# Kernel optimization log

Hardware: AMD Instinct MI355X
Metric: run time of the kernel (lower is better)

The kernel has to match this reference:

```python
import jax, jax.numpy as jnp
import numpy as np

VOCAB = 32000; DIM = 512; NL = 6; B = 2; L = 1024
DI = 2 * DIM      # d_inner (expand=2)
DS = 16           # d_state
DC = 4            # d_conv
DR = DIM // 16    # dt_rank = ceil(512/16) = 32


def setup_inputs() -> dict:
    key = jax.random.key(0)
    ks = jax.random.split(key, 10)
    s = 0.02
    tokens = jax.random.randint(ks[0], (B, L), 0, VOCAB)
    pos_emb = jax.random.normal(ks[1], (1, L, DIM)) * s
    embed = jax.random.normal(ks[2], (VOCAB, DIM)) * s
    lm_w = jax.random.normal(ks[3], (VOCAB, DIM)) * s
    lm_b = jnp.zeros((VOCAB,), jnp.float32)
    in_proj_w = jax.random.normal(ks[4], (NL, 2 * DI, DIM)) * s
    conv_w = jax.random.normal(ks[5], (NL, DI, DC)) * s
    conv_b = jnp.zeros((NL, DI), jnp.float32)
    x_proj_w = jax.random.normal(ks[6], (NL, DR + 2 * DS, DI)) * s
    dt_proj_w = jax.random.normal(ks[7], (NL, DI, DR)) * s
    dt_proj_b = jnp.broadcast_to(jnp.log(jnp.expm1(jnp.float32(0.01))), (NL, DI)).astype(jnp.float32)
    A_log = jnp.log(jnp.broadcast_to(jnp.arange(1, DS + 1, dtype=jnp.float32), (NL, DI, DS)))
    Dp = jnp.ones((NL, DI), jnp.float32)
    out_w = jax.random.normal(ks[8], (NL, DIM, DI)) * s
    ln_g = jnp.ones((NL, DIM), jnp.float32)
    ln_b = jnp.zeros((NL, DIM), jnp.float32)
    return dict(tokens=tokens, pos_emb=pos_emb, embed=embed, lm_w=lm_w, lm_b=lm_b,
                in_proj_w=in_proj_w, conv_w=conv_w, conv_b=conv_b, x_proj_w=x_proj_w,
                dt_proj_w=dt_proj_w, dt_proj_b=dt_proj_b, A_log=A_log, Dp=Dp,
                out_w=out_w, ln_g=ln_g, ln_b=ln_b)


def silu(x):
    return x * jax.nn.sigmoid(x)


def layernorm(x, g, b, eps=1e-5):
    mu = jnp.mean(x, -1, keepdims=True)
    var = jnp.var(x, -1, keepdims=True)
    return (x - mu) * jax.lax.rsqrt(var + eps) * g + b


def causal_dwconv(x, w, b):
    # x: (B,L,DI), w: (DI,DC) depthwise, left-pad causal
    xp = jnp.pad(x, ((0, 0), (DC - 1, 0), (0, 0)))
    y = b
    for k in range(DC):
        y = y + w[:, k] * xp[:, k:k + x.shape[1], :]
    return y


def selective_scan(u, dt, A, Bm, Cm, Dp):
    # u,dt: (B,L,DI); A: (DI,DS); Bm,Cm: (B,L,DS)
    dA = jnp.exp(dt[..., None] * A)                       # (B,L,DI,DS)
    dBu = dt[..., None] * Bm[:, :, None, :] * u[..., None]
    h0 = jnp.zeros((u.shape[0], DI, DS), u.dtype)

    def step(h, inp):
        dA_t, dBu_t, C_t = inp
        h = dA_t * h + dBu_t
        y = jnp.einsum('bdn,bn->bd', h, C_t)
        return h, y

    _, ys = jax.lax.scan(step, h0, (dA.transpose(1, 0, 2, 3),
                                    dBu.transpose(1, 0, 2, 3),
                                    Cm.transpose(1, 0, 2)))
    return ys.transpose(1, 0, 2) + u * Dp


def mamba_block(x, in_w, cw, cb, xp_w, dtw, dtb, A_log, Dp, ow):
    xz = jnp.einsum('bld,ed->ble', x, in_w)               # (B,L,2*DI)
    xc, z = jnp.split(xz, 2, axis=-1)
    xc = silu(causal_dwconv(xc, cw, cb))
    x_dbl = jnp.einsum('bld,ed->ble', xc, xp_w)           # (B,L,DR+2*DS)
    dt, Bm, Cm = jnp.split(x_dbl, [DR, DR + DS], axis=-1)
    dt = jax.nn.softplus(jnp.einsum('blr,dr->bld', dt, dtw) + dtb)
    A = -jnp.exp(A_log)
    y = selective_scan(xc, dt, A, Bm, Cm, Dp)
    y = y * silu(z)
    return jnp.einsum('bld,ed->ble', y, ow)


def reference(tokens, pos_emb, embed, lm_w, lm_b, in_proj_w, conv_w, conv_b,
              x_proj_w, dt_proj_w, dt_proj_b, A_log, Dp, out_w, ln_g, ln_b):
    x = embed[tokens] + pos_emb[:, :tokens.shape[1]]
    for i in range(NL):
        res = x
        x = mamba_block(x, in_proj_w[i], conv_w[i], conv_b[i], x_proj_w[i],
                        dt_proj_w[i], dt_proj_b[i], A_log[i], Dp[i], out_w[i])
        x = layernorm(x + res, ln_g[i], ln_b[i])
    return jnp.einsum('bld,vd->blv', x, lm_w) + lm_b
```

## Files before the change

kernel.cpp:

```cpp
#include <hip/hip_runtime.h>
#include <hip/hip_bf16.h>
#include <math.h>

#define BB 2
#define LL 1024
#define DIM 512
#define NL 6
#define DI 1024
#define DS 16
#define DC 4
#define DR 32
#define VOCAB 32000
#define M_ROWS (BB * LL)
#define CCH 64
#define CHLEN (LL / CCH)
#define KSPLIT 8
#define OSPLIT 4

typedef unsigned short u16;
typedef __attribute__((ext_vector_type(8))) short bf16x8;
typedef __attribute__((ext_vector_type(4))) float f32x4;

__device__ __forceinline__ u16 f2bf(float f) {
    unsigned u = __float_as_uint(f);
    u += 0x7FFF + ((u >> 16) & 1);
    return (u16)(u >> 16);
}
__device__ __forceinline__ float bf2f(u16 h) {
    return __uint_as_float(((unsigned)h) << 16);
}
#define SWZ(r, c) ((c) ^ (((r) >> 1) & 3))

__global__ __launch_bounds__(256) void cast_all(const float* __restrict__ lm,
                                                const float* __restrict__ inw,
                                                const float* __restrict__ ow,
                                                const float* __restrict__ xp,
                                                u16* __restrict__ lmb,
                                                u16* __restrict__ inb,
                                                u16* __restrict__ owb_,
                                                u16* __restrict__ xpb) {
    int idx = blockIdx.x * 256 + threadIdx.x;
    const float* src; u16* dst; int off;
    if (idx < 2048000)      { src = lm;  dst = lmb;  off = idx; }
    else if (idx < 2834432) { src = inw; dst = inb;  off = idx - 2048000; }
    else if (idx < 3227648) { src = ow;  dst = owb_; off = idx - 2834432; }
    else                    { src = xp;  dst = xpb;  off = idx - 3227648; }
    float4 v0 = ((const float4*)src)[off * 2];
    float4 v1 = ((const float4*)src)[off * 2 + 1];
    union { u16 h[8]; int4 v; } r;
    r.h[0] = f2bf(v0.x); r.h[1] = f2bf(v0.y); r.h[2] = f2bf(v0.z); r.h[3] = f2bf(v0.w);
    r.h[4] = f2bf(v1.x); r.h[5] = f2bf(v1.y); r.h[6] = f2bf(v1.z); r.h[7] = f2bf(v1.w);
    ((int4*)dst)[off] = r.v;
}

__global__ __launch_bounds__(256) void embed_kernel(const int* __restrict__ tok,
                                                    const float* __restrict__ pos,
                                                    const float* __restrict__ emb,
                                                    float* __restrict__ x,
                                                    u16* __restrict__ xb) {
    int idx = blockIdx.x * 256 + threadIdx.x;
    int d = idx & (DIM - 1);
    int l = (idx >> 9) & (LL - 1);
    int b = idx >> 19;
    int t = tok[b * LL + l];
    float v = emb[(size_t)t * DIM + d] + pos[l * DIM + d];
    x[idx] = v;
    xb[idx] = f2bf(v);
}

__global__ __launch_bounds__(256) void gemm_bf16(const u16* __restrict__ A,
                                                 const u16* __restrict__ W,
                                                 const float* __restrict__ bias,
                                                 float* __restrict__ C,
                                                 int M, int N, int K,
                                                 int lda, int ldw) {
    __shared__ __align__(16) u16 As[2 * 4096];
    __shared__ __align__(16) u16 Ws[2 * 4096];
    const int t = threadIdx.x;
    const int l = t & 63;
    const int w = t >> 6;
    const int nwg = gridDim.x;
    const int q = nwg >> 3, r8 = nwg & 7;
    const int xcd = blockIdx.x & 7, rank = blockIdx.x >> 3;
    const int wgid = (xcd < r8 ? xcd * (q + 1) : r8 * (q + 1) + (xcd - r8) * q) + rank;
    const int Mb = M >> 7;
    const int bm = (wgid % Mb) * 128;
    const int bn = (wgid / Mb) * 128;
    const int wm = (w >> 1) * 64;
    const int wn = (w & 1) * 64;

    f32x4 acc[4][4] = {};
    const int nt = K >> 5;

    auto STAGE = [&](int bufi, int k0) {
#pragma unroll
        for (int p = 0; p < 2; ++p) {
            const int i = (p * 4 + w) * 64 + l;
            const int row = i >> 2;
            const int kq = SWZ(row, i & 3);
            __builtin_amdgcn_global_load_lds(
                (const __attribute__((address_space(1))) unsigned int*)
                    (A + (size_t)(bm + row) * lda + k0 + kq * 8),
                (__attribute__((address_space(3))) unsigned int*)
                    (As + bufi * 4096 + (p * 4 + w) * 512),
                16, 0, 0);
            __builtin_amdgcn_global_load_lds(
                (const __attribute__((address_space(1))) unsigned int*)
                    (W + (size_t)(bn + row) * ldw + k0 + kq * 8),
                (__attribute__((address_space(3))) unsigned int*)
                    (Ws + bufi * 4096 + (p * 4 + w) * 512),
                16, 0, 0);
        }
    };
    auto COMPUTE = [&](int bufi) {
        const u16* Ab = As + bufi * 4096;
        const u16* Wb = Ws + bufi * 4096;
#pragma unroll
        for (int mi = 0; mi < 4; ++mi) {
            const int ar = wm + mi * 16 + (l & 15);
            bf16x8 a = *(const bf16x8*)(Ab + ar * 32 + SWZ(ar, l >> 4) * 8);
#pragma unroll
            for (int ni = 0; ni < 4; ++ni) {
                const int wr = wn + ni * 16 + (l & 15);
                bf16x8 b = *(const bf16x8*)(Wb + wr * 32 + SWZ(wr, l >> 4) * 8);
                acc[mi][ni] = __builtin_amdgcn_mfma_f32_16x16x32_bf16(b, a, acc[mi][ni], 0, 0, 0);
            }
        }
    };

    STAGE(0, 0);
    for (int tt = 0; tt < nt; ++tt) {
        if (tt + 1 < nt) {
            STAGE((tt + 1) & 1, (tt + 1) << 5);
            asm volatile("s_waitcnt vmcnt(4)\ns_barrier" ::: "memory");
        } else {
            asm volatile("s_waitcnt vmcnt(0)\ns_barrier" ::: "memory");
        }
        COMPUTE(tt & 1);
        asm volatile("s_waitcnt lgkmcnt(0)\ns_barrier" ::: "memory");
    }

#pragma unroll
    for (int mi = 0; mi < 4; ++mi) {
        const int row = bm + wm + mi * 16 + (l & 15);
#pragma unroll
        for (int ni = 0; ni < 4; ++ni) {
            const int col = bn + wn + ni * 16 + ((l >> 4) << 2);
            float4 v;
            v.x = acc[mi][ni][0]; v.y = acc[mi][ni][1];
            v.z = acc[mi][ni][2]; v.w = acc[mi][ni][3];
            if (bias != nullptr) {
                float4 b4 = *(const float4*)(bias + col);
                v.x += b4.x; v.y += b4.y; v.z += b4.z; v.w += b4.w;
            }
            *(float4*)(C + (size_t)row * N + col) = v;
        }
    }
}

__global__ __launch_bounds__(256) void gemm_n64(const u16* __restrict__ A,
                                                const u16* __restrict__ W,
                                                float* __restrict__ out,
                                                u16* __restrict__ outb,
                                                int lda, int ldw, int ldc,
                                                int KS, int pstride) {
    __shared__ __align__(16) u16 As[2 * 4096];
    __shared__ __align__(16) u16 Ws[2 * 2048];
    const int t = threadIdx.x;
    const int l = t & 63;
    const int w = t >> 6;
    const int kz = blockIdx.x;
    const int bm = blockIdx.y * 128;
    const int bnn = blockIdx.z * 64;
    const int wm = w * 32;

    f32x4 acc[2][4] = {};
    const int nt = KS >> 5;
    const int kbeg = kz * KS;

    auto STAGE = [&](int bufi, int k0) {
#pragma unroll
        for (int p = 0; p < 2; ++p) {
            const int i = p * 256 + w * 64 + l;
            const int row = i >> 2;
            const int kq = SWZ(row, i & 3);
            __builtin_amdgcn_global_load_lds(
                (const __attribute__((address_space(1))) unsigned int*)
                    (A + (size_t)(bm + row) * lda + k0 + kq * 8),
                (__attribute__((address_space(3))) unsigned int*)
                    (As + bufi * 4096 + (p * 256 + w * 64) * 8),
                16, 0, 0);
        }
        {
            const int i = w * 64 + l;
            const int row = i >> 2;
            const int kq = SWZ(row, i & 3);
            __builtin_amdgcn_global_load_lds(
                (const __attribute__((address_space(1))) unsigned int*)
                    (W + (size_t)(bnn + row) * ldw + k0 + kq * 8),
                (__attribute__((address_space(3))) unsigned int*)
                    (Ws + bufi * 2048 + (w * 64) * 8),
                16, 0, 0);
        }
    };
    auto COMPUTE = [&](int bufi) {
        const u16* Ab = As + bufi * 4096;
        const u16* Wb = Ws + bufi * 2048;
#pragma unroll
        for (int mi = 0; mi < 2; ++mi) {
            const int ar = wm + mi * 16 + (l & 15);
            bf16x8 a = *(const bf16x8*)(Ab + ar * 32 + SWZ(ar, l >> 4) * 8);
#pragma unroll
            for (int ni = 0; ni < 4; ++ni) {
                const int wr = ni * 16 + (l & 15);
                bf16x8 b = *(const bf16x8*)(Wb + wr * 32 + SWZ(wr, l >> 4) * 8);
                acc[mi][ni] = __builtin_amdgcn_mfma_f32_16x16x32_bf16(b, a, acc[mi][ni], 0, 0, 0);
            }
        }
    };

    STAGE(0, kbeg);
    for (int tt = 0; tt < nt; ++tt) {
        if (tt + 1 < nt) {
            STAGE((tt + 1) & 1, kbeg + ((tt + 1) << 5));
            asm volatile("s_waitcnt vmcnt(3)\ns_barrier" ::: "memory");
        } else {
            asm volatile("s_waitcnt vmcnt(0)\ns_barrier" ::: "memory");
        }
        COMPUTE(tt & 1);
        asm volatile("s_waitcnt lgkmcnt(0)\ns_barrier" ::: "memory");
    }

    if (outb != nullptr) {
        u16* opb = outb + (size_t)kz * pstride;
#pragma unroll
        for (int mi = 0; mi < 2; ++mi) {
            const int row = bm + wm + mi * 16 + (l & 15);
#pragma unroll
            for (int ni = 0; ni < 4; ++ni) {
                const int col = bnn + ni * 16 + ((l >> 4) << 2);
                ushort4 v;
                v.x = f2bf(acc[mi][ni][0]); v.y = f2bf(acc[mi][ni][1]);
                v.z = f2bf(acc[mi][ni][2]); v.w = f2bf(acc[mi][ni][3]);
                *(ushort4*)(opb + (size_t)row * ldc + col) = v;
            }
        }
    } else {
        float* op = out + (size_t)kz * pstride;
#pragma unroll
        for (int mi = 0; mi < 2; ++mi) {
            const int row = bm + wm + mi * 16 + (l & 15);
#pragma unroll
            for (int ni = 0; ni < 4; ++ni) {
                const int col = bnn + ni * 16 + ((l >> 4) << 2);
                float4 v;
                v.x = acc[mi][ni][0]; v.y = acc[mi][ni][1];
                v.z = acc[mi][ni][2]; v.w = acc[mi][ni][3];
                *(float4*)(op + (size_t)row * ldc + col) = v;
            }
        }
    }
}

__global__ __launch_bounds__(256) void xdred_dt(const float* __restrict__ Pf,
                                                const float* __restrict__ dtw,
                                                const float* __restrict__ dtb,
                                                float* __restrict__ xd,
                                                float* __restrict__ dt) {
    __shared__ float xds[64];
    const int m = blockIdx.x;
    const int t = threadIdx.x;
    if (t < 64) {
        float s = 0.f;
#pragma unroll
        for (int kz = 0; kz < KSPLIT; ++kz)
            s += Pf[(size_t)kz * (M_ROWS * 64) + m * 64 + t];
        xds[t] = s;
        xd[m * 64 + t] = s;
    }
    __syncthreads();
    const int d0 = t * 4;
    const float4 bv = *(const float4*)(dtb + d0);
    float a0 = bv.x, a1 = bv.y, a2 = bv.z, a3 = bv.w;
    const float* w0p = dtw + (size_t)(d0 + 0) * DR;
    const float* w1p = dtw + (size_t)(d0 + 1) * DR;
    const float* w2p = dtw + (size_t)(d0 + 2) * DR;
    const float* w3p = dtw + (size_t)(d0 + 3) * DR;
#pragma unroll
    for (int k = 0; k < DR; k += 4) {
        float4 xv = *(const float4*)&xds[k];
        float4 w0 = *(const float4*)(w0p + k);
        float4 w1 = *(const float4*)(w1p + k);
        float4 w2 = *(const float4*)(w2p + k);
        float4 w3 = *(const float4*)(w3p + k);
        a0 += w0.x * xv.x + w0.y * xv.y + w0.z * xv.z + w0.w * xv.w;
        a1 += w1.x * xv.x + w1.y * xv.y + w1.z * xv.z + w1.w * xv.w;
        a2 += w2.x * xv.x + w2.y * xv.y + w2.z * xv.z + w2.w * xv.w;
        a3 += w3.x * xv.x + w3.y * xv.y + w3.z * xv.z + w3.w * xv.w;
    }
    a0 = (a0 > 20.f) ? a0 : log1pf(__expf(a0));
    a1 = (a1 > 20.f) ? a1 : log1pf(__expf(a1));
    a2 = (a2 > 20.f) ? a2 : log1pf(__expf(a2));
    a3 = (a3 > 20.f) ? a3 : log1pf(__expf(a3));
    float4 v; v.x = a0; v.y = a1; v.z = a2; v.w = a3;
    *(float4*)(dt + (size_t)m * DI + d0) = v;
}

__global__ __launch_bounds__(256) void conv_silu(const u16* __restrict__ xzb,
                                                 const float* __restrict__ cw,
                                                 const float* __restrict__ cb,
                                                 float* __restrict__ xc,
                                                 u16* __restrict__ xcb) {
    int idx = blockIdx.x * 256 + threadIdx.x;
    int c = idx & (DI - 1);
    int l = (idx >> 10) & (LL - 1);
    int b = idx >> 20;
    float acc = cb[c];
#pragma unroll
    for (int k = 0; k < DC; ++k) {
        int ll = l + k - (DC - 1);
        if (ll >= 0)
            acc += cw[c * DC + k] * bf2f(xzb[((size_t)(b * LL + ll)) * (2 * DI) + c]);
    }
    float v = acc / (1.f + __expf(-acc));
    xc[idx] = v;
    xcb[idx] = f2bf(v);
}

__global__ __launch_bounds__(256) void scan_pass1(const float* __restrict__ xc,
                                                  const float* __restrict__ dt,
                                                  const float* __restrict__ xdbl,
                                                  const float* __restrict__ A_log,
                                                  float* __restrict__ S,
                                                  float* __restrict__ Q) {
    const int d = blockIdx.x * 256 + threadIdx.x;
    const int b = blockIdx.y;
    const int c = blockIdx.z;
    float a[DS];
#pragma unroll
    for (int q = 0; q < 4; ++q) {
        float4 al = *(const float4*)(A_log + d * DS + q * 4);
        a[q * 4 + 0] = -__expf(al.x);
        a[q * 4 + 1] = -__expf(al.y);
        a[q * 4 + 2] = -__expf(al.z);
        a[q * 4 + 3] = -__expf(al.w);
    }
    float Qr[DS];
#pragma unroll
    for (int n = 0; n < DS; ++n) Qr[n] = 0.f;
    float Ssum = 0.f;

    const int l0 = c * CHLEN;
    const float* dtp = dt + ((size_t)b * LL + l0) * DI + d;
    const float* up  = xc + ((size_t)b * LL + l0) * DI + d;
    const float* xdp = xdbl + ((size_t)b * LL + l0) * 64 + DR;

    for (int l = 0; l < CHLEN; ++l) {
        float dtv = dtp[(size_t)l * DI];
        float uv  = up[(size_t)l * DI];
        float wv = dtv * uv;
        Ssum += dtv;
#pragma unroll
        for (int q = 0; q < 4; ++q) {
            float4 Bv = *(const float4*)(xdp + l * 64 + q * 4);
            float dA0 = __expf(dtv * a[q * 4 + 0]);
            float dA1 = __expf(dtv * a[q * 4 + 1]);
            float dA2 = __expf(dtv * a[q * 4 + 2]);
            float dA3 = __expf(dtv * a[q * 4 + 3]);
            Qr[q * 4 + 0] = dA0 * Qr[q * 4 + 0] + wv * Bv.x;
            Qr[q * 4 + 1] = dA1 * Qr[q * 4 + 1] + wv * Bv.y;
            Qr[q * 4 + 2] = dA2 * Qr[q * 4 + 2] + wv * Bv.z;
            Qr[q * 4 + 3] = dA3 * Qr[q * 4 + 3] + wv * Bv.w;
        }
    }
    S[((size_t)b * CCH + c) * DI + d] = Ssum;
    float* Qp = Q + (((size_t)b * CCH + c) * DI + d) * DS;
#pragma unroll
    for (int q = 0; q < 4; ++q) {
        float4 o;
        o.x = Qr[q * 4 + 0]; o.y = Qr[q * 4 + 1];
        o.z = Qr[q * 4 + 2]; o.w = Qr[q * 4 + 3];
        *(float4*)(Qp + q * 4) = o;
    }
}

__global__ __launch_bounds__(64) void scan_pass2(const float* __restrict__ A_log,
                                                 const float* __restrict__ S,
                                                 float* __restrict__ Q) {
    const int idx = blockIdx.x * 64 + threadIdx.x;
    const int b = idx >> 14;
    const int dn = idx & 16383;
    const int d = dn >> 4;
    const float a = -__expf(A_log[dn]);
    float h = 0.f;
    for (int c = 0; c < CCH; ++c) {
        const size_t soff = ((size_t)b * CCH + c) * DI + d;
        const size_t qoff = ((size_t)b * CCH + c) * (size_t)(DI * DS) + dn;
        float P = __expf(a * S[soff]);
        float qv = Q[qoff];
        Q[qoff] = h;
        h = P * h + qv;
    }
}

__global__ __launch_bounds__(256) void scan_pass3(const float* __restrict__ xc,
                                                  const float* __restrict__ dt,
                                                  const float* __restrict__ xdbl,
                                                  const u16* __restrict__ xzb,
                                                  const float* __restrict__ A_log,
                                                  const float* __restrict__ Dpp,
                                                  const float* __restrict__ Q,
                                                  u16* __restrict__ y) {
    const int d = blockIdx.x * 256 + threadIdx.x;
    const int b = blockIdx.y;
    const int c = blockIdx.z;
    float a[DS];
#pragma unroll
    for (int q = 0; q < 4; ++q) {
        float4 al = *(const float4*)(A_log + d * DS + q * 4);
        a[q * 4 + 0] = -__expf(al.x);
        a[q * 4 + 1] = -__expf(al.y);
        a[q * 4 + 2] = -__expf(al.z);
        a[q * 4 + 3] = -__expf(al.w);
    }
    float h[DS];
    const float* Qp = Q + (((size_t)b * CCH + c) * DI + d) * DS;
#pragma unroll
    for (int q = 0; q < 4; ++q) {
        float4 hv = *(const float4*)(Qp + q * 4);
        h[q * 4 + 0] = hv.x; h[q * 4 + 1] = hv.y;
        h[q * 4 + 2] = hv.z; h[q * 4 + 3] = hv.w;
    }
    const float dp = Dpp[d];

    const int l0 = c * CHLEN;
    const float* dtp = dt + ((size_t)b * LL + l0) * DI + d;
    const float* up  = xc + ((size_t)b * LL + l0) * DI + d;
    const float* xdp = xdbl + ((size_t)b * LL + l0) * 64 + DR;
    const u16* zp = xzb + ((size_t)b * LL + l0) * (2 * DI) + DI + d;
    u16* yp = y + ((size_t)b * LL + l0) * DI + d;

    for (int l = 0; l < CHLEN; ++l) {
        float dtv = dtp[(size_t)l * DI];
        float uv  = up[(size_t)l * DI];
        float wv = dtv * uv;
        float p = 0.f;
#pragma unroll
        for (int q = 0; q < 4; ++q) {
            float4 Bv = *(const float4*)(xdp + l * 64 + q * 4);
            float4 Cv = *(const float4*)(xdp + l * 64 + 16 + q * 4);
            float dA0 = __expf(dtv * a[q * 4 + 0]);
            float dA1 = __expf(dtv * a[q * 4 + 1]);
            float dA2 = __expf(dtv * a[q * 4 + 2]);
            float dA3 = __expf(dtv * a[q * 4 + 3]);
            h[q * 4 + 0] = dA0 * h[q * 4 + 0] + wv * Bv.x;
            h[q * 4 + 1] = dA1 * h[q * 4 + 1] + wv * Bv.y;
            h[q * 4 + 2] = dA2 * h[q * 4 + 2] + wv * Bv.z;
            h[q * 4 + 3] = dA3 * h[q * 4 + 3] + wv * Bv.w;
            p += h[q * 4 + 0] * Cv.x + h[q * 4 + 1] * Cv.y +
                 h[q * 4 + 2] * Cv.z + h[q * 4 + 3] * Cv.w;
        }
        float zv = bf2f(zp[(size_t)l * (2 * DI)]);
        float g = zv / (1.f + __expf(-zv));
        yp[(size_t)l * DI] = f2bf((p + uv * dp) * g);
    }
}

__global__ __launch_bounds__(256) void add_ln(const float* __restrict__ opart,
                                              float* __restrict__ x,
                                              const float* __restrict__ g,
                                              const float* __restrict__ b,
                                              u16* __restrict__ xb) {
    const int PS = M_ROWS * DIM;
    int m = blockIdx.x;
    int t = threadIdx.x;
    const float* xr = x + (size_t)m * DIM;
    float v0 = xr[t];
    float v1 = xr[t + 256];
#pragma unroll
    for (int kz = 0; kz < OSPLIT; ++kz) {
        const float* op = opart + (size_t)kz * PS + (size_t)m * DIM;
        v0 += op[t];
        v1 += op[t + 256];
    }
    float s = v0 + v1;
    float ss = v0 * v0 + v1 * v1;
#pragma unroll
    for (int off = 32; off > 0; off >>= 1) {
        s += __shfl_down(s, off, 64);
        ss += __shfl_down(ss, off, 64);
    }
    __shared__ float sb[4], ssb[4];
    int w = t >> 6;
    if ((t & 63) == 0) { sb[w] = s; ssb[w] = ss; }
    __syncthreads();
    float stot = sb[0] + sb[1] + sb[2] + sb[3];
    float sstot = ssb[0] + ssb[1] + ssb[2] + ssb[3];
    float mean = stot * (1.f / DIM);
    float var = sstot * (1.f / DIM) - mean * mean;
    float rs = rsqrtf(var + 1e-5f);
    float* xw = x + (size_t)m * DIM;
    float o0 = (v0 - mean) * rs * g[t] + b[t];
    float o1 = (v1 - mean) * rs * g[t + 256] + b[t + 256];
    xw[t] = o0;
    xw[t + 256] = o1;
    xb[(size_t)m * DIM + t] = f2bf(o0);
    xb[(size_t)m * DIM + t + 256] = f2bf(o1);
}

extern "C" void kernel_launch(void* const* d_in, const int* in_sizes, int n_in,
                              void* d_out, int out_size, void* d_ws, size_t ws_size,
                              hipStream_t stream) {
    const int*   tokens = (const int*)d_in[0];
    const float* pos    = (const float*)d_in[1];
    const float* emb    = (const float*)d_in[2];
    const float* lm_w   = (const float*)d_in[3];
    const float* lm_b   = (const float*)d_in[4];
    const float* in_w   = (const float*)d_in[5];
    const float* cw     = (const float*)d_in[6];
    const float* cb     = (const float*)d_in[7];
    const float* xpw    = (const float*)d_in[8];
    const float* dtw    = (const float*)d_in[9];
    const float* dtb    = (const float*)d_in[10];
    const float* A_log  = (const float*)d_in[11];
    const float* Dpp    = (const float*)d_in[12];
    const float* ow     = (const float*)d_in[13];
    const float* lng    = (const float*)d_in[14];
    const float* lnb    = (const float*)d_in[15];
    float* out = (float*)d_out;

    float* ws = (float*)d_ws;
    float* x    = ws;
    float* xc   = x + 1048576;
    float* xd   = xc + 2097152;
    float* dt   = xd + 131072;
    float* S    = dt + 2097152;
    float* Qb   = S + 131072;
    float* Pf   = Qb + 2097152;
    float* Pf2  = Pf + 1048576;
    u16* xzb    = (u16*)(Pf2 + 4194304);
    u16* xb     = xzb + 4194304;
    u16* yb     = xb + 1048576;
    u16* xcb    = yb + 2097152;
    u16* lm_wb  = xcb + 2097152;
    u16* in_wb  = lm_wb + 16384000;
    u16* owb    = in_wb + 6291456;
    u16* xpwb   = owb + 3145728;

    cast_all<<<12800, 256, 0, stream>>>(lm_w, in_w, ow, xpw,
                                        lm_wb, in_wb, owb, xpwb);

    embed_kernel<<<M_ROWS * DIM / 256, 256, 0, stream>>>(tokens, pos, emb, x, xb);

    for (int i = 0; i < NL; ++i) {
        gemm_n64<<<dim3(1, M_ROWS / 128, 2048 / 64), 256, 0, stream>>>(
            xb, in_wb + (size_t)i * 2048 * 512, nullptr, xzb,
            512, 512, 2048, 512, 0);
        conv_silu<<<M_ROWS * DI / 256, 256, 0, stream>>>(
            xzb, cw + (size_t)i * DI * DC, cb + (size_t)i * DI, xc, xcb);
        gemm_n64<<<dim3(KSPLIT, M_ROWS / 128, 1), 256, 0, stream>>>(
            xcb, xpwb + (size_t)i * 64 * 1024, Pf, nullptr,
            1024, 1024, 64, 1024 / KSPLIT, M_ROWS * 64);
        xdred_dt<<<M_ROWS, 256, 0, stream>>>(
            Pf, dtw + (size_t)i * DI * DR, dtb + (size_t)i * DI, xd, dt);
        scan_pass1<<<dim3(DI / 256, BB, CCH), 256, 0, stream>>>(
            xc, dt, xd, A_log + (size_t)i * DI * DS, S, Qb);
        scan_pass2<<<(BB * DI * DS) / 64, 64, 0, stream>>>(
            A_log + (size_t)i * DI * DS, S, Qb);
        scan_pass3<<<dim3(DI / 256, BB, CCH), 256, 0, stream>>>(
            xc, dt, xd, xzb, A_log + (size_t)i * DI * DS, Dpp + (size_t)i * DI, Qb, yb);
        gemm_n64<<<dim3(OSPLIT, M_ROWS / 128, 512 / 64), 256, 0, stream>>>(
            yb, owb + (size_t)i * 512 * 1024, Pf2, nullptr,
            1024, 1024, 512, 1024 / OSPLIT, M_ROWS * 512);
        add_ln<<<M_ROWS, 256, 0, stream>>>(
            Pf2, x, lng + (size_t)i * DIM, lnb + (size_t)i * DIM, xb);
    }

    gemm_bf16<<<(VOCAB / 128) * (M_ROWS / 128), 256, 0, stream>>>(
        xb, lm_wb, lm_b, out, M_ROWS, VOCAB, 512, 512, 512);
}
```

Measured before the change: 838.1 us.

## Drop fp32 conv output and run LM head through gemm_n64 with bias

```diff
diff --git a/kernel.cpp b/kernel.cpp
--- a/kernel.cpp
+++ b/kernel.cpp
@@ -68,100 +68,11 @@
     xb[idx] = f2bf(v);
 }
 
-__global__ __launch_bounds__(256) void gemm_bf16(const u16* __restrict__ A,
-                                                 const u16* __restrict__ W,
-                                                 const float* __restrict__ bias,
-                                                 float* __restrict__ C,
-                                                 int M, int N, int K,
-                                                 int lda, int ldw) {
-    __shared__ __align__(16) u16 As[2 * 4096];
-    __shared__ __align__(16) u16 Ws[2 * 4096];
-    const int t = threadIdx.x;
-    const int l = t & 63;
-    const int w = t >> 6;
-    const int nwg = gridDim.x;
-    const int q = nwg >> 3, r8 = nwg & 7;
-    const int xcd = blockIdx.x & 7, rank = blockIdx.x >> 3;
-    const int wgid = (xcd < r8 ? xcd * (q + 1) : r8 * (q + 1) + (xcd - r8) * q) + rank;
-    const int Mb = M >> 7;
-    const int bm = (wgid % Mb) * 128;
-    const int bn = (wgid / Mb) * 128;
-    const int wm = (w >> 1) * 64;
-    const int wn = (w & 1) * 64;
-
-    f32x4 acc[4][4] = {};
-    const int nt = K >> 5;
-
-    auto STAGE = [&](int bufi, int k0) {
-#pragma unroll
-        for (int p = 0; p < 2; ++p) {
-            const int i = (p * 4 + w) * 64 + l;
-            const int row = i >> 2;
-            const int kq = SWZ(row, i & 3);
-            __builtin_amdgcn_global_load_lds(
-                (const __attribute__((address_space(1))) unsigned int*)
-                    (A + (size_t)(bm + row) * lda + k0 + kq * 8),
-                (__attribute__((address_space(3))) unsigned int*)
-                    (As + bufi * 4096 + (p * 4 + w) * 512),
-                16, 0, 0);
-            __builtin_amdgcn_global_load_lds(
-                (const __attribute__((address_space(1))) unsigned int*)
-                    (W + (size_t)(bn + row) * ldw + k0 + kq * 8),
-                (__attribute__((address_space(3))) unsigned int*)
-                    (Ws + bufi * 4096 + (p * 4 + w) * 512),
-                16, 0, 0);
-        }
-    };
-    auto COMPUTE = [&](int bufi) {
-        const u16* Ab = As + bufi * 4096;
-        const u16* Wb = Ws + bufi * 4096;
-#pragma unroll
-        for (int mi = 0; mi < 4; ++mi) {
-            const int ar = wm + mi * 16 + (l & 15);
-            bf16x8 a = *(const bf16x8*)(Ab + ar * 32 + SWZ(ar, l >> 4) * 8);
-#pragma unroll
-            for (int ni = 0; ni < 4; ++ni) {
-                const int wr = wn + ni * 16 + (l & 15);
-                bf16x8 b = *(const bf16x8*)(Wb + wr * 32 + SWZ(wr, l >> 4) * 8);
-                acc[mi][ni] = __builtin_amdgcn_mfma_f32_16x16x32_bf16(b, a, acc[mi][ni], 0, 0, 0);
-            }
-        }
-    };
-
-    STAGE(0, 0);
-    for (int tt = 0; tt < nt; ++tt) {
-        if (tt + 1 < nt) {
-            STAGE((tt + 1) & 1, (tt + 1) << 5);
-            asm volatile("s_waitcnt vmcnt(4)\ns_barrier" ::: "memory");
-        } else {
-            asm volatile("s_waitcnt vmcnt(0)\ns_barrier" ::: "memory");
-        }
-        COMPUTE(tt & 1);
-        asm volatile("s_waitcnt lgkmcnt(0)\ns_barrier" ::: "memory");
-    }
-
-#pragma unroll
-    for (int mi = 0; mi < 4; ++mi) {
-        const int row = bm + wm + mi * 16 + (l & 15);
-#pragma unroll
-        for (int ni = 0; ni < 4; ++ni) {
-            const int col = bn + wn + ni * 16 + ((l >> 4) << 2);
-            float4 v;
-            v.x = acc[mi][ni][0]; v.y = acc[mi][ni][1];
-            v.z = acc[mi][ni][2]; v.w = acc[mi][ni][3];
-            if (bias != nullptr) {
-                float4 b4 = *(const float4*)(bias + col);
-                v.x += b4.x; v.y += b4.y; v.z += b4.z; v.w += b4.w;
-            }
-            *(float4*)(C + (size_t)row * N + col) = v;
-        }
-    }
-}
-
 __global__ __launch_bounds__(256) void gemm_n64(const u16* __restrict__ A,
                                                 const u16* __restrict__ W,
                                                 float* __restrict__ out,
                                                 u16* __restrict__ outb,
+                                                const float* __restrict__ bias,
                                                 int lda, int ldw, int ldc,
                                                 int KS, int pstride) {
     __shared__ __align__(16) u16 As[2 * 4096];
@@ -256,6 +167,10 @@
                 float4 v;
                 v.x = acc[mi][ni][0]; v.y = acc[mi][ni][1];
                 v.z = acc[mi][ni][2]; v.w = acc[mi][ni][3];
+                if (bias != nullptr) {
+                    float4 b4 = *(const float4*)(bias + col);
+                    v.x += b4.x; v.y += b4.y; v.z += b4.z; v.w += b4.w;
+                }
                 *(float4*)(op + (size_t)row * ldc + col) = v;
             }
         }
@@ -309,7 +224,6 @@
 __global__ __launch_bounds__(256) void conv_silu(const u16* __restrict__ xzb,
                                                  const float* __restrict__ cw,
                                                  const float* __restrict__ cb,
-                                                 float* __restrict__ xc,
                                                  u16* __restrict__ xcb) {
     int idx = blockIdx.x * 256 + threadIdx.x;
     int c = idx & (DI - 1);
@@ -323,11 +237,10 @@
             acc += cw[c * DC + k] * bf2f(xzb[((size_t)(b * LL + ll)) * (2 * DI) + c]);
     }
     float v = acc / (1.f + __expf(-acc));
-    xc[idx] = v;
     xcb[idx] = f2bf(v);
 }
 
-__global__ __launch_bounds__(256) void scan_pass1(const float* __restrict__ xc,
+__global__ __launch_bounds__(256) void scan_pass1(const u16* __restrict__ xcb,
                                                   const float* __restrict__ dt,
                                                   const float* __restrict__ xdbl,
                                                   const float* __restrict__ A_log,
@@ -352,12 +265,12 @@
 
     const int l0 = c * CHLEN;
     const float* dtp = dt + ((size_t)b * LL + l0) * DI + d;
-    const float* up  = xc + ((size_t)b * LL + l0) * DI + d;
+    const u16*   up  = xcb + ((size_t)b * LL + l0) * DI + d;
     const float* xdp = xdbl + ((size_t)b * LL + l0) * 64 + DR;
 
     for (int l = 0; l < CHLEN; ++l) {
         float dtv = dtp[(size_t)l * DI];
-        float uv  = up[(size_t)l * DI];
+        float uv  = bf2f(up[(size_t)l * DI]);
         float wv = dtv * uv;
         Ssum += dtv;
 #pragma unroll
@@ -403,7 +316,7 @@
     }
 }
 
-__global__ __launch_bounds__(256) void scan_pass3(const float* __restrict__ xc,
+__global__ __launch_bounds__(256) void scan_pass3(const u16* __restrict__ xcb,
                                                   const float* __restrict__ dt,
                                                   const float* __restrict__ xdbl,
                                                   const u16* __restrict__ xzb,
@@ -435,14 +348,14 @@
 
     const int l0 = c * CHLEN;
     const float* dtp = dt + ((size_t)b * LL + l0) * DI + d;
-    const float* up  = xc + ((size_t)b * LL + l0) * DI + d;
+    const u16*   up  = xcb + ((size_t)b * LL + l0) * DI + d;
     const float* xdp = xdbl + ((size_t)b * LL + l0) * 64 + DR;
     const u16* zp = xzb + ((size_t)b * LL + l0) * (2 * DI) + DI + d;
     u16* yp = y + ((size_t)b * LL + l0) * DI + d;
 
     for (int l = 0; l < CHLEN; ++l) {
         float dtv = dtp[(size_t)l * DI];
-        float uv  = up[(size_t)l * DI];
+        float uv  = bf2f(up[(size_t)l * DI]);
         float wv = dtv * uv;
         float p = 0.f;
 #pragma unroll
@@ -531,8 +444,7 @@
 
     float* ws = (float*)d_ws;
     float* x    = ws;
-    float* xc   = x + 1048576;
-    float* xd   = xc + 2097152;
+    float* xd   = x + 1048576;
     float* dt   = xd + 131072;
     float* S    = dt + 2097152;
     float* Qb   = S + 131072;
@@ -554,28 +466,29 @@
 
     for (int i = 0; i < NL; ++i) {
         gemm_n64<<<dim3(1, M_ROWS / 128, 2048 / 64), 256, 0, stream>>>(
-            xb, in_wb + (size_t)i * 2048 * 512, nullptr, xzb,
+            xb, in_wb + (size_t)i * 2048 * 512, nullptr, xzb, nullptr,
             512, 512, 2048, 512, 0);
         conv_silu<<<M_ROWS * DI / 256, 256, 0, stream>>>(
-            xzb, cw + (size_t)i * DI * DC, cb + (size_t)i * DI, xc, xcb);
+            xzb, cw + (size_t)i * DI * DC, cb + (size_t)i * DI, xcb);
         gemm_n64<<<dim3(KSPLIT, M_ROWS / 128, 1), 256, 0, stream>>>(
-            xcb, xpwb + (size_t)i * 64 * 1024, Pf, nullptr,
+            xcb, xpwb + (size_t)i * 64 * 1024, Pf, nullptr, nullptr,
             1024, 1024, 64, 1024 / KSPLIT, M_ROWS * 64);
         xdred_dt<<<M_ROWS, 256, 0, stream>>>(
             Pf, dtw + (size_t)i * DI * DR, dtb + (size_t)i * DI, xd, dt);
         scan_pass1<<<dim3(DI / 256, BB, CCH), 256, 0, stream>>>(
-            xc, dt, xd, A_log + (size_t)i * DI * DS, S, Qb);
+            xcb, dt, xd, A_log + (size_t)i * DI * DS, S, Qb);
         scan_pass2<<<(BB * DI * DS) / 64, 64, 0, stream>>>(
             A_log + (size_t)i * DI * DS, S, Qb);
         scan_pass3<<<dim3(DI / 256, BB, CCH), 256, 0, stream>>>(
-            xc, dt, xd, xzb, A_log + (size_t)i * DI * DS, Dpp + (size_t)i * DI, Qb, yb);
+            xcb, dt, xd, xzb, A_log + (size_t)i * DI * DS, Dpp + (size_t)i * DI, Qb, yb);
         gemm_n64<<<dim3(OSPLIT, M_ROWS / 128, 512 / 64), 256, 0, stream>>>(
-            yb, owb + (size_t)i * 512 * 1024, Pf2, nullptr,
+            yb, owb + (size_t)i * 512 * 1024, Pf2, nullptr, nullptr,
             1024, 1024, 512, 1024 / OSPLIT, M_ROWS * 512);
         add_ln<<<M_ROWS, 256, 0, stream>>>(
             Pf2, x, lng + (size_t)i * DIM, lnb + (size_t)i * DIM, xb);
     }
 
-    gemm_bf16<<<(VOCAB / 128) * (M_ROWS / 128), 256, 0, stream>>>(
-        xb, lm_wb, lm_b, out, M_ROWS, VOCAB, 512, 512, 512);
-}
+    gemm_n64<<<dim3(1, M_ROWS / 128, VOCAB / 64), 256, 0, stream>>>(
+        xb, lm_wb, out, nullptr, lm_b,
+        512, 512, VOCAB, 512, 0);
+}
```

New measurement: 841.8 us. Within noise of the previous version (+0.4%).
